# Optimization experiments

Measured on AMD Instinct MI355X. Metric: run time of the kernel, lower is better.

## Reference

```python
import jax, jax.numpy as jnp
import numpy as np

N_NODES = 50000
N_EDGES = 600000
N_FEAT = 128
NHID = 128
N_CLASSES = 10
N_GRAPHS = 512
BN_EPS = 1e-5


def _gcn_conv(x, W, b, src, dst, n):
    """PyG GCNConv: D^{-1/2}(A+I)D^{-1/2} X W + b (symmetric norm, self-loops)."""
    xw = x @ W  # [n, out]
    deg = jax.ops.segment_sum(jnp.ones(src.shape[0], x.dtype), dst, num_segments=n) + 1.0
    dinv = jax.lax.rsqrt(deg)  # [n]
    norm = dinv[src] * dinv[dst]  # [E]
    agg = jax.ops.segment_sum(xw[src] * norm[:, None], dst, num_segments=n)
    agg = agg + xw * (dinv * dinv)[:, None]  # self-loop contribution
    return agg + b


def setup_inputs() -> dict:
    key = jax.random.key(0)
    ks = jax.random.split(key, 16)
    s_in = 1.0 / np.sqrt(N_FEAT)
    s_h = 1.0 / np.sqrt(NHID)
    s_h2 = 1.0 / np.sqrt(NHID // 2)
    return {
        "x": jax.random.normal(ks[0], (N_NODES, N_FEAT), jnp.float32),
        "edge_index": jax.random.randint(ks[1], (2, N_EDGES), 0, N_NODES, jnp.int32),
        "batch": jnp.sort(jax.random.randint(ks[2], (N_NODES,), 0, N_GRAPHS, jnp.int32)),
        "W1": jax.random.normal(ks[3], (N_FEAT, NHID), jnp.float32) * s_in,
        "b1": jnp.zeros((NHID,), jnp.float32),
        "W2": jax.random.normal(ks[4], (NHID, NHID), jnp.float32) * s_h,
        "b2": jnp.zeros((NHID,), jnp.float32),
        "W3": jax.random.normal(ks[5], (NHID, NHID), jnp.float32) * s_h,
        "b3": jnp.zeros((NHID,), jnp.float32),
        "gamma": jnp.ones((NHID,), jnp.float32),
        "beta": jnp.zeros((NHID,), jnp.float32),
        "run_mean": jnp.zeros((NHID,), jnp.float32),
        "run_var": jnp.ones((NHID,), jnp.float32),
        "lw1": jax.random.normal(ks[6], (NHID, NHID), jnp.float32) * s_h,
        "lb1": jnp.zeros((NHID,), jnp.float32),
        "lw2": jax.random.normal(ks[7], (NHID, NHID // 2), jnp.float32) * s_h,
        "lb2": jnp.zeros((NHID // 2,), jnp.float32),
        "lw3": jax.random.normal(ks[8], (NHID // 2, N_CLASSES), jnp.float32) * s_h2,
        "lb3": jnp.zeros((N_CLASSES,), jnp.float32),
    }


def reference(x, edge_index, batch, W1, b1, W2, b2, W3, b3,
              gamma, beta, run_mean, run_var,
              lw1, lb1, lw2, lb2, lw3, lb3):
    src, dst = edge_index[0], edge_index[1]
    h = jax.nn.relu(_gcn_conv(x, W1, b1, src, dst, N_NODES))
    h = jax.nn.relu(_gcn_conv(h, W2, b2, src, dst, N_NODES))
    h = jax.nn.relu(_gcn_conv(h, W3, b3, src, dst, N_NODES))
    # BatchNorm1d (eval: running stats)
    h = (h - run_mean) * jax.lax.rsqrt(run_var + BN_EPS) * gamma + beta
    # scatter_max over graph ids -> [N_GRAPHS, NHID]
    g = jax.ops.segment_max(h, batch, num_segments=N_GRAPHS)
    g = jax.nn.relu(g @ lw1 + lb1)
    g = jax.nn.relu(g @ lw2 + lb2)
    return g @ lw3 + lb3
```

## Files before the change

### kernel.cpp

```cpp
#include <hip/hip_runtime.h>
#include <hip/hip_bf16.h>

#define NHID 128
#define NGRAPH 512
#define NCLS 10

typedef __attribute__((ext_vector_type(8))) short bf16x8;
typedef __attribute__((ext_vector_type(4))) float f32x4;
typedef __attribute__((ext_vector_type(4))) unsigned int u32x4;

__device__ inline unsigned int fenc(float f) {
    unsigned int u = __float_as_uint(f);
    return (u & 0x80000000u) ? ~u : (u | 0x80000000u);
}
__device__ inline float fdec(unsigned int u) {
    u = (u & 0x80000000u) ? (u & 0x7fffffffu) : ~u;
    return __uint_as_float(u);
}
__device__ inline unsigned short f2bf(float f) {
    unsigned int u = __float_as_uint(f);
    return (unsigned short)((u + 0x7fffu + ((u >> 16) & 1u)) >> 16);
}
__device__ inline unsigned int packbf(float lo, float hi) {
    return (unsigned)f2bf(lo) | ((unsigned)f2bf(hi) << 16);
}

__global__ void k_front(const int* __restrict__ dst, int* __restrict__ cnt, int E, int degB,
                        const float* __restrict__ x, unsigned int* __restrict__ xb, int n8, int xB,
                        const float* __restrict__ W1, const float* __restrict__ W2,
                        const float* __restrict__ W3, unsigned short* __restrict__ Wt,
                        unsigned int* __restrict__ keys) {
    int b = blockIdx.x;
    if (b < degB) {
        int e = b * 256 + threadIdx.x;
        if (e < E) atomicAdd(&cnt[dst[e]], 1);
    } else if (b < degB + xB) {
        int i = (b - degB) * 256 + threadIdx.x;
        if (i < n8) {
            const float* p = x + (size_t)i * 8;
            f32x4 a = *reinterpret_cast<const f32x4*>(p);
            f32x4 c = *reinterpret_cast<const f32x4*>(p + 4);
            u32x4 o;
            o[0] = packbf(a[0], a[1]);
            o[1] = packbf(a[2], a[3]);
            o[2] = packbf(c[0], c[1]);
            o[3] = packbf(c[2], c[3]);
            *reinterpret_cast<u32x4*>(xb + (size_t)i * 4) = o;
        }
    } else if (b < degB + xB + 192) {
        int idx = (b - degB - xB) * 256 + threadIdx.x;
        int l = idx >> 14;
        int r = idx & 16383;
        const float* W = (l == 0) ? W1 : (l == 1) ? W2 : W3;
        int c = r & 127, k = r >> 7;
        Wt[l * 16384 + c * NHID + k] = f2bf(W[k * NHID + c]);
    } else {
        int i = (b - degB - xB - 192) * 256 + threadIdx.x;
        if (i < NGRAPH * NHID) keys[i] = 0u;
    }
}

__global__ __launch_bounds__(1024) void k_scan1(const int* __restrict__ cnt,
        float* __restrict__ dinv, int* __restrict__ rowptr,
        int* __restrict__ bsum, int N) {
    __shared__ int lds[1024];
    int t = threadIdx.x;
    int i = blockIdx.x * 1024 + t;
    int v = (i < N) ? cnt[i] : 0;
    if (i < N) dinv[i] = rsqrtf((float)v + 1.0f);
    lds[t] = v;
    __syncthreads();
    for (int off = 1; off < 1024; off <<= 1) {
        int x = (t >= off) ? lds[t - off] : 0;
        __syncthreads();
        lds[t] += x;
        __syncthreads();
    }
    if (i < N) rowptr[i] = lds[t] - v;
    if (t == 1023) bsum[blockIdx.x] = lds[1023];
}

__global__ __launch_bounds__(1024) void k_scan2(int* __restrict__ bsum, int nb) {
    __shared__ int lds[1024];
    int t = threadIdx.x;
    int v = (t < nb) ? bsum[t] : 0;
    lds[t] = v;
    __syncthreads();
    for (int off = 1; off < 1024; off <<= 1) {
        int x = (t >= off) ? lds[t - off] : 0;
        __syncthreads();
        lds[t] += x;
        __syncthreads();
    }
    if (t < nb) bsum[t] = lds[t] - v;
}

__global__ void k_fill(const int* __restrict__ src, const int* __restrict__ dst,
                       const int* __restrict__ rowptr, const int* __restrict__ bsum,
                       int* __restrict__ cursor, int* __restrict__ csr_src, int E) {
    int e = blockIdx.x * blockDim.x + threadIdx.x;
    if (e >= E) return;
    int s = src[e], d = dst[e];
    int pos = rowptr[d] + bsum[d >> 10] + atomicAdd(&cursor[d], 1);
    csr_src[pos] = s;
}

__device__ inline void fma8(const u32x4& u, float nw, float* a) {
#pragma unroll
    for (int q = 0; q < 4; ++q) {
        a[2 * q]     = fmaf(nw, __uint_as_float(u[q] << 16), a[2 * q]);
        a[2 * q + 1] = fmaf(nw, __uint_as_float(u[q] & 0xffff0000u), a[2 * q + 1]);
    }
}

__global__ __launch_bounds__(256) void k_agg(const unsigned int* __restrict__ Hb,
        const int* __restrict__ csr_src, const int* __restrict__ rowptr,
        const int* __restrict__ bsum, const int* __restrict__ cnt,
        const float* __restrict__ dinv, unsigned int* __restrict__ aggb, int N) {
    int w = (blockIdx.x * 256 + threadIdx.x) >> 6;
    if (w >= N) return;
    int lane = threadIdx.x & 63;
    int g = lane >> 4;
    int l16 = lane & 15;
    float diw = dinv[w];
    u32x4 us = reinterpret_cast<const u32x4*>(Hb + (size_t)w * (NHID / 2))[l16];
    float a[8];
#pragma unroll
    for (int e = 0; e < 8; ++e) a[e] = 0.f;
    int beg = rowptr[w] + bsum[w >> 10];
    int deg = cnt[w];
    int end = beg + deg;
    int trips = (deg + 15) >> 4;
    int j = beg + g;
    for (int t = 0; t < trips; ++t, j += 16) {
        int s0 = w, s1 = w, s2 = w, s3 = w;
        if (j < end)      s0 = csr_src[j];
        if (j + 4 < end)  s1 = csr_src[j + 4];
        if (j + 8 < end)  s2 = csr_src[j + 8];
        if (j + 12 < end) s3 = csr_src[j + 12];
        float n0 = (j < end)      ? dinv[s0] * diw : 0.f;
        float n1 = (j + 4 < end)  ? dinv[s1] * diw : 0.f;
        float n2 = (j + 8 < end)  ? dinv[s2] * diw : 0.f;
        float n3 = (j + 12 < end) ? dinv[s3] * diw : 0.f;
        u32x4 u0 = reinterpret_cast<const u32x4*>(Hb + (size_t)s0 * (NHID / 2))[l16];
        u32x4 u1 = reinterpret_cast<const u32x4*>(Hb + (size_t)s1 * (NHID / 2))[l16];
        u32x4 u2 = reinterpret_cast<const u32x4*>(Hb + (size_t)s2 * (NHID / 2))[l16];
        u32x4 u3 = reinterpret_cast<const u32x4*>(Hb + (size_t)s3 * (NHID / 2))[l16];
        fma8(u0, n0, a);
        fma8(u1, n1, a);
        fma8(u2, n2, a);
        fma8(u3, n3, a);
    }
    if (g == 0) fma8(us, diw * diw, a);
#pragma unroll
    for (int e = 0; e < 8; ++e) {
        a[e] += __shfl_xor(a[e], 16);
        a[e] += __shfl_xor(a[e], 32);
    }
    if (g == 0) {
        u32x4 o;
        o[0] = packbf(a[0], a[1]);
        o[1] = packbf(a[2], a[3]);
        o[2] = packbf(a[4], a[5]);
        o[3] = packbf(a[6], a[7]);
        *reinterpret_cast<u32x4*>(aggb + (size_t)w * (NHID / 2) + l16 * 4) = o;
    }
}

__global__ __launch_bounds__(256) void k_gemm(const unsigned short* __restrict__ A,
        const unsigned short* __restrict__ Wt, const float* __restrict__ bias,
        unsigned short* __restrict__ Hb, int M) {
    int wave = threadIdx.x >> 6;
    int lane = threadIdx.x & 63;
    int lr = lane & 15;
    int kq = lane >> 4;
    int r0 = blockIdx.x * 64 + wave * 16;
    f32x4 acc[8];
#pragma unroll
    for (int nt = 0; nt < 8; ++nt) acc[nt] = 0.f;
    int ar = r0 + lr;
    bool arok = ar < M;
#pragma unroll
    for (int kg = 0; kg < 4; ++kg) {
        int kb = kg * 32 + kq * 8;
        bf16x8 af = bf16x8(0);
        if (arok) af = *reinterpret_cast<const bf16x8*>(A + (size_t)ar * NHID + kb);
#pragma unroll
        for (int nt = 0; nt < 8; ++nt) {
            bf16x8 bf = *reinterpret_cast<const bf16x8*>(Wt + (size_t)(nt * 16 + lr) * NHID + kb);
            acc[nt] = __builtin_amdgcn_mfma_f32_16x16x32_bf16(af, bf, acc[nt], 0, 0, 0);
        }
    }
#pragma unroll
    for (int nt = 0; nt < 8; ++nt) {
        int c = nt * 16 + lr;
        float b = bias[c];
#pragma unroll
        for (int e = 0; e < 4; ++e) {
            int r = r0 + kq * 4 + e;
            if (r < M) {
                float v = fmaxf(acc[nt][e] + b, 0.f);
                Hb[(size_t)r * NHID + c] = f2bf(v);
            }
        }
    }
}

__global__ __launch_bounds__(256) void k_gemm_bn(const unsigned short* __restrict__ A,
        const unsigned short* __restrict__ Wt, const float* __restrict__ bias,
        const int* __restrict__ batch, const float* __restrict__ gamma,
        const float* __restrict__ beta, const float* __restrict__ rmean,
        const float* __restrict__ rvar, unsigned int* __restrict__ keys, int M) {
    __shared__ unsigned int smax[64][NHID];
    __shared__ int bseg[64];
    int tid = threadIdx.x;
    int n0 = blockIdx.x * 64;
    for (int i = tid; i < 64 * NHID; i += 256) ((unsigned int*)smax)[i] = 0u;
    if (tid < 64) {
        int r = n0 + tid;
        bseg[tid] = batch[r < M ? r : M - 1];
    }
    int wave = tid >> 6;
    int lane = tid & 63;
    int lr = lane & 15;
    int kq = lane >> 4;
    int r0 = n0 + wave * 16;
    f32x4 acc[8];
#pragma unroll
    for (int nt = 0; nt < 8; ++nt) acc[nt] = 0.f;
    int ar = r0 + lr;
    bool arok = ar < M;
#pragma unroll
    for (int kg = 0; kg < 4; ++kg) {
        int kb = kg * 32 + kq * 8;
        bf16x8 af = bf16x8(0);
        if (arok) af = *reinterpret_cast<const bf16x8*>(A + (size_t)ar * NHID + kb);
#pragma unroll
        for (int nt = 0; nt < 8; ++nt) {
            bf16x8 bf = *reinterpret_cast<const bf16x8*>(Wt + (size_t)(nt * 16 + lr) * NHID + kb);
            acc[nt] = __builtin_amdgcn_mfma_f32_16x16x32_bf16(af, bf, acc[nt], 0, 0, 0);
        }
    }
    __syncthreads();
    int glo = bseg[0];
#pragma unroll
    for (int nt = 0; nt < 8; ++nt) {
        int c = nt * 16 + lr;
        float b = bias[c];
        float sc = gamma[c] * rsqrtf(rvar[c] + 1e-5f);
        float sh = beta[c] - rmean[c] * sc;
#pragma unroll
        for (int e = 0; e < 4; ++e) {
            int rr = wave * 16 + kq * 4 + e;
            if (n0 + rr < M) {
                float v = fmaxf(acc[nt][e] + b, 0.f);
                float y = fmaf(v, sc, sh);
                atomicMax(&smax[bseg[rr] - glo][c], fenc(y));
            }
        }
    }
    __syncthreads();
    int last = M - 1 - n0;
    if (last > 63) last = 63;
    int span = bseg[last] - glo + 1;
    for (int i = tid; i < span * NHID; i += 256) {
        unsigned int v = ((unsigned int*)smax)[i];
        if (v) atomicMax(&keys[(size_t)(glo + (i >> 7)) * NHID + (i & 127)], v);
    }
}

__global__ __launch_bounds__(128) void k_head(const unsigned int* __restrict__ keys,
        const float* __restrict__ lw1, const float* __restrict__ lb1,
        const float* __restrict__ lw2, const float* __restrict__ lb2,
        const float* __restrict__ lw3, const float* __restrict__ lb3,
        float* __restrict__ out) {
    __shared__ float g0[NHID], g1[NHID], g2[64];
    int r = blockIdx.x;
    int t = threadIdx.x;
    unsigned int u = keys[(size_t)r * NHID + t];
    g0[t] = (u == 0u) ? -3.0e38f : fdec(u);
    __syncthreads();
    float acc = lb1[t];
#pragma unroll 8
    for (int k = 0; k < NHID; ++k) acc = fmaf(g0[k], lw1[k * NHID + t], acc);
    g1[t] = fmaxf(acc, 0.f);
    __syncthreads();
    if (t < 64) {
        acc = lb2[t];
#pragma unroll 8
        for (int k = 0; k < NHID; ++k) acc = fmaf(g1[k], lw2[k * 64 + t], acc);
        g2[t] = fmaxf(acc, 0.f);
    }
    __syncthreads();
    if (t < NCLS) {
        acc = lb3[t];
#pragma unroll 8
        for (int k = 0; k < 64; ++k) acc = fmaf(g2[k], lw3[k * NCLS + t], acc);
        out[(size_t)r * NCLS + t] = acc;
    }
}

extern "C" void kernel_launch(void* const* d_in, const int* in_sizes, int n_in,
                              void* d_out, int out_size, void* d_ws, size_t ws_size,
                              hipStream_t stream) {
    const float* x     = (const float*)d_in[0];
    const int*   ei    = (const int*)d_in[1];
    const int*   batch = (const int*)d_in[2];
    const float* W1 = (const float*)d_in[3];
    const float* b1 = (const float*)d_in[4];
    const float* W2 = (const float*)d_in[5];
    const float* b2 = (const float*)d_in[6];
    const float* W3 = (const float*)d_in[7];
    const float* b3 = (const float*)d_in[8];
    const float* gamma = (const float*)d_in[9];
    const float* beta  = (const float*)d_in[10];
    const float* rmean = (const float*)d_in[11];
    const float* rvar  = (const float*)d_in[12];
    const float* lw1 = (const float*)d_in[13];
    const float* lb1 = (const float*)d_in[14];
    const float* lw2 = (const float*)d_in[15];
    const float* lb2 = (const float*)d_in[16];
    const float* lw3 = (const float*)d_in[17];
    const float* lb3 = (const float*)d_in[18];

    const int N = in_sizes[2];
    const int E = in_sizes[1] / 2;
    const int* src = ei;
    const int* dst = ei + E;

    char* ws = (char*)d_ws;
    size_t off = 0;
    auto alloc = [&](size_t bytes) {
        char* p = ws + off;
        off += (bytes + 255) & ~(size_t)255;
        return p;
    };
    int*   cnt     = (int*)  alloc((size_t)N * 8);
    int*   cursor  = cnt + N;
    int*   rowptr  = (int*)  alloc((size_t)N * 4);
    int*   bsum    = (int*)  alloc(1024 * 4);
    float* dinv    = (float*)alloc((size_t)N * 4);
    int*   csr_src = (int*)  alloc((size_t)E * 4);
    unsigned int* xb   = (unsigned int*)alloc((size_t)N * NHID * 2);
    unsigned int* aggb = (unsigned int*)alloc((size_t)N * NHID * 2);
    unsigned int* Hb   = (unsigned int*)alloc((size_t)N * NHID * 2);
    unsigned short* Wt = (unsigned short*)alloc((size_t)3 * NHID * NHID * 2);
    unsigned int* keys = (unsigned int*)alloc((size_t)NGRAPH * NHID * 4);
    (void)ws_size; (void)n_in; (void)out_size;

    hipMemsetAsync(cnt, 0, (size_t)N * 8, stream);

    int degB = (E + 255) / 256;
    int n8 = N * 16;
    int xB = (n8 + 255) / 256;
    int frontB = degB + xB + 192 + (NGRAPH * NHID + 255) / 256;
    k_front<<<frontB, 256, 0, stream>>>(dst, cnt, E, degB, x, xb, n8, xB,
                                        W1, W2, W3, Wt, keys);
    int nb1 = (N + 1023) / 1024;
    k_scan1<<<nb1, 1024, 0, stream>>>(cnt, dinv, rowptr, bsum, N);
    k_scan2<<<1, 1024, 0, stream>>>(bsum, nb1);
    k_fill<<<degB, 256, 0, stream>>>(src, dst, rowptr, bsum, cursor, csr_src, E);

    int ab = ((size_t)N * 64 + 255) / 256;
    int gb = (N + 63) / 64;
    k_agg<<<ab, 256, 0, stream>>>(xb, csr_src, rowptr, bsum, cnt, dinv, aggb, N);
    k_gemm<<<gb, 256, 0, stream>>>((const unsigned short*)aggb, Wt, b1, (unsigned short*)Hb, N);
    k_agg<<<ab, 256, 0, stream>>>(Hb, csr_src, rowptr, bsum, cnt, dinv, aggb, N);
    k_gemm<<<gb, 256, 0, stream>>>((const unsigned short*)aggb, Wt + 16384, b2, (unsigned short*)Hb, N);
    k_agg<<<ab, 256, 0, stream>>>(Hb, csr_src, rowptr, bsum, cnt, dinv, aggb, N);
    k_gemm_bn<<<gb, 256, 0, stream>>>((const unsigned short*)aggb, Wt + 32768, b3,
                                      batch, gamma, beta, rmean, rvar, keys, N);

    k_head<<<NGRAPH, 128, 0, stream>>>(keys, lw1, lb1, lw2, lb2, lw3, lb3, (float*)d_out);
}
```

Before: 248.9 us.

## Fuse neighbor aggregation with following GEMM for first two GCN layers

Adds a k_agg_gemm kernel where 16 waves each aggregate one node's neighbors into LDS, then 8 waves run a 16x128x128 MFMA with bias and ReLU on that tile. It replaces the separate agg and gemm launches for layers 1 and 2, so the aggregated intermediate no longer makes a global-memory round trip and two launches are dropped. The cost is 1024-thread blocks with a barrier, which can leave waves idle behind the slowest high-degree node. The GEMM phase also uses only half the waves, and each block reloads the full weight matrix for just 16 rows.

Result: faster. 234.9 us (-5.6%).

```diff
diff --git a/kernel.cpp b/kernel.cpp
--- a/kernel.cpp
+++ b/kernel.cpp
@@ -110,6 +110,90 @@
     for (int q = 0; q < 4; ++q) {
         a[2 * q]     = fmaf(nw, __uint_as_float(u[q] << 16), a[2 * q]);
         a[2 * q + 1] = fmaf(nw, __uint_as_float(u[q] & 0xffff0000u), a[2 * q + 1]);
+    }
+}
+
+__global__ __launch_bounds__(1024) void k_agg_gemm(const unsigned int* __restrict__ Hin,
+        const int* __restrict__ csr_src, const int* __restrict__ rowptr,
+        const int* __restrict__ bsum, const int* __restrict__ cnt,
+        const float* __restrict__ dinv, const unsigned short* __restrict__ Wt,
+        const float* __restrict__ bias, unsigned short* __restrict__ Hout, int N) {
+    __shared__ unsigned int lds[16][68];
+    int wv = threadIdx.x >> 6;
+    int lane = threadIdx.x & 63;
+    int g = lane >> 4;
+    int l16 = lane & 15;
+    int w = blockIdx.x * 16 + wv;
+    if (w < N) {
+        float diw = dinv[w];
+        u32x4 us = reinterpret_cast<const u32x4*>(Hin + (size_t)w * (NHID / 2))[l16];
+        float a[8];
+#pragma unroll
+        for (int e = 0; e < 8; ++e) a[e] = 0.f;
+        int beg = rowptr[w] + bsum[w >> 10];
+        int deg = cnt[w];
+        int end = beg + deg;
+        int trips = (deg + 15) >> 4;
+        int j = beg + g;
+        for (int t = 0; t < trips; ++t, j += 16) {
+            int s0 = w, s1 = w, s2 = w, s3 = w;
+            if (j < end)      s0 = csr_src[j];
+            if (j + 4 < end)  s1 = csr_src[j + 4];
+            if (j + 8 < end)  s2 = csr_src[j + 8];
+            if (j + 12 < end) s3 = csr_src[j + 12];
+            float n0 = (j < end)      ? dinv[s0] * diw : 0.f;
+            float n1 = (j + 4 < end)  ? dinv[s1] * diw : 0.f;
+            float n2 = (j + 8 < end)  ? dinv[s2] * diw : 0.f;
+            float n3 = (j + 12 < end) ? dinv[s3] * diw : 0.f;
+            u32x4 u0 = reinterpret_cast<const u32x4*>(Hin + (size_t)s0 * (NHID / 2))[l16];
+            u32x4 u1 = reinterpret_cast<const u32x4*>(Hin + (size_t)s1 * (NHID / 2))[l16];
+            u32x4 u2 = reinterpret_cast<const u32x4*>(Hin + (size_t)s2 * (NHID / 2))[l16];
+            u32x4 u3 = reinterpret_cast<const u32x4*>(Hin + (size_t)s3 * (NHID / 2))[l16];
+            fma8(u0, n0, a);
+            fma8(u1, n1, a);
+            fma8(u2, n2, a);
+            fma8(u3, n3, a);
+        }
+        if (g == 0) fma8(us, diw * diw, a);
+#pragma unroll
+        for (int e = 0; e < 8; ++e) {
+            a[e] += __shfl_xor(a[e], 16);
+            a[e] += __shfl_xor(a[e], 32);
+        }
+        if (g == 0) {
+            u32x4 o;
+            o[0] = packbf(a[0], a[1]);
+            o[1] = packbf(a[2], a[3]);
+            o[2] = packbf(a[4], a[5]);
+            o[3] = packbf(a[6], a[7]);
+            *reinterpret_cast<u32x4*>(&lds[wv][l16 * 4]) = o;
+        }
+    } else if (g == 0) {
+        u32x4 z = {0u, 0u, 0u, 0u};
+        *reinterpret_cast<u32x4*>(&lds[wv][l16 * 4]) = z;
+    }
+    __syncthreads();
+    if (wv < 8) {
+        int lr = l16;
+        int kq = g;
+        f32x4 acc = {0.f, 0.f, 0.f, 0.f};
+#pragma unroll
+        for (int kg = 0; kg < 4; ++kg) {
+            bf16x8 af = *reinterpret_cast<const bf16x8*>(&lds[lr][kg * 16 + kq * 4]);
+            bf16x8 bf = *reinterpret_cast<const bf16x8*>(
+                Wt + (size_t)(wv * 16 + lr) * NHID + kg * 32 + kq * 8);
+            acc = __builtin_amdgcn_mfma_f32_16x16x32_bf16(af, bf, acc, 0, 0, 0);
+        }
+        int c = wv * 16 + lr;
+        float b = bias[c];
+#pragma unroll
+        for (int e = 0; e < 4; ++e) {
+            int r = blockIdx.x * 16 + kq * 4 + e;
+            if (r < N) {
+                float v = fmaxf(acc[e] + b, 0.f);
+                Hout[(size_t)r * NHID + c] = f2bf(v);
+            }
+        }
     }
 }
 
@@ -167,45 +251,6 @@
     }
 }
 
-__global__ __launch_bounds__(256) void k_gemm(const unsigned short* __restrict__ A,
-        const unsigned short* __restrict__ Wt, const float* __restrict__ bias,
-        unsigned short* __restrict__ Hb, int M) {
-    int wave = threadIdx.x >> 6;
-    int lane = threadIdx.x & 63;
-    int lr = lane & 15;
-    int kq = lane >> 4;
-    int r0 = blockIdx.x * 64 + wave * 16;
-    f32x4 acc[8];
-#pragma unroll
-    for (int nt = 0; nt < 8; ++nt) acc[nt] = 0.f;
-    int ar = r0 + lr;
-    bool arok = ar < M;
-#pragma unroll
-    for (int kg = 0; kg < 4; ++kg) {
-        int kb = kg * 32 + kq * 8;
-        bf16x8 af = bf16x8(0);
-        if (arok) af = *reinterpret_cast<const bf16x8*>(A + (size_t)ar * NHID + kb);
-#pragma unroll
-        for (int nt = 0; nt < 8; ++nt) {
-            bf16x8 bf = *reinterpret_cast<const bf16x8*>(Wt + (size_t)(nt * 16 + lr) * NHID + kb);
-            acc[nt] = __builtin_amdgcn_mfma_f32_16x16x32_bf16(af, bf, acc[nt], 0, 0, 0);
-        }
-    }
-#pragma unroll
-    for (int nt = 0; nt < 8; ++nt) {
-        int c = nt * 16 + lr;
-        float b = bias[c];
-#pragma unroll
-        for (int e = 0; e < 4; ++e) {
-            int r = r0 + kq * 4 + e;
-            if (r < M) {
-                float v = fmaxf(acc[nt][e] + b, 0.f);
-                Hb[(size_t)r * NHID + c] = f2bf(v);
-            }
-        }
-    }
-}
-
 __global__ __launch_bounds__(256) void k_gemm_bn(const unsigned short* __restrict__ A,
         const unsigned short* __restrict__ Wt, const float* __restrict__ bias,
         const int* __restrict__ batch, const float* __restrict__ gamma,
@@ -342,8 +387,8 @@
     float* dinv    = (float*)alloc((size_t)N * 4);
     int*   csr_src = (int*)  alloc((size_t)E * 4);
     unsigned int* xb   = (unsigned int*)alloc((size_t)N * NHID * 2);
-    unsigned int* aggb = (unsigned int*)alloc((size_t)N * NHID * 2);
     unsigned int* Hb   = (unsigned int*)alloc((size_t)N * NHID * 2);
+    unsigned int* H2   = (unsigned int*)alloc((size_t)N * NHID * 2);
     unsigned short* Wt = (unsigned short*)alloc((size_t)3 * NHID * NHID * 2);
     unsigned int* keys = (unsigned int*)alloc((size_t)NGRAPH * NHID * 4);
     (void)ws_size; (void)n_in; (void)out_size;
@@ -361,14 +406,15 @@
     k_scan2<<<1, 1024, 0, stream>>>(bsum, nb1);
     k_fill<<<degB, 256, 0, stream>>>(src, dst, rowptr, bsum, cursor, csr_src, E);
 
+    int fgb = (N + 15) / 16;
     int ab = ((size_t)N * 64 + 255) / 256;
     int gb = (N + 63) / 64;
-    k_agg<<<ab, 256, 0, stream>>>(xb, csr_src, rowptr, bsum, cnt, dinv, aggb, N);
-    k_gemm<<<gb, 256, 0, stream>>>((const unsigned short*)aggb, Wt, b1, (unsigned short*)Hb, N);
-    k_agg<<<ab, 256, 0, stream>>>(Hb, csr_src, rowptr, bsum, cnt, dinv, aggb, N);
-    k_gemm<<<gb, 256, 0, stream>>>((const unsigned short*)aggb, Wt + 16384, b2, (unsigned short*)Hb, N);
-    k_agg<<<ab, 256, 0, stream>>>(Hb, csr_src, rowptr, bsum, cnt, dinv, aggb, N);
-    k_gemm_bn<<<gb, 256, 0, stream>>>((const unsigned short*)aggb, Wt + 32768, b3,
+    k_agg_gemm<<<fgb, 1024, 0, stream>>>(xb, csr_src, rowptr, bsum, cnt, dinv,
+                                         Wt, b1, (unsigned short*)Hb, N);
+    k_agg_gemm<<<fgb, 1024, 0, stream>>>(Hb, csr_src, rowptr, bsum, cnt, dinv,
+                                         Wt + 16384, b2, (unsigned short*)H2, N);
+    k_agg<<<ab, 256, 0, stream>>>(H2, csr_src, rowptr, bsum, cnt, dinv, Hb, N);
+    k_gemm_bn<<<gb, 256, 0, stream>>>((const unsigned short*)Hb, Wt + 32768, b3,
                                       batch, gamma, beta, rmean, rvar, keys, N);
 
     k_head<<<NGRAPH, 128, 0, stream>>>(keys, lw1, lb1, lw2, lb2, lw3, lb3, (float*)d_out);
```
